# Kernel tuning notes

Hardware: AMD Instinct MI355X
Metric: run time of the kernel (lower is better)

The kernel has to match this reference:

```python
import jax, jax.numpy as jnp
import numpy as np
from jax import lax

K = 3          # kernel size
PAD = 1        # (K-1)//2
CIN = 256
COUT = 64
NSPLIT = CIN // COUT  # 4
EPS = 1e-5


def _conv2d(x, w, b):
    # x [B,C,H,W], w [O,I,K,K], b [O]
    y = lax.conv_general_dilated(x, w, (1, 1), [(PAD, PAD), (PAD, PAD)],
                                 dimension_numbers=("NCHW", "OIHW", "NCHW"))
    return y + b[None, :, None, None]


def _bilinear_sample(img, py, px):
    # img [C,H,W]; py,px [K2,H,W] absolute sample coords; zero outside borders
    H, W = img.shape[1], img.shape[2]
    y0 = jnp.floor(py)
    x0 = jnp.floor(px)
    wy1 = py - y0
    wx1 = px - x0
    wy0 = 1.0 - wy1
    wx0 = 1.0 - wx1

    def gather(yc, xc):
        valid = (yc >= 0) & (yc <= H - 1) & (xc >= 0) & (xc <= W - 1)
        yi = jnp.clip(yc, 0, H - 1).astype(jnp.int32)
        xi = jnp.clip(xc, 0, W - 1).astype(jnp.int32)
        v = img[:, yi, xi]  # [C,K2,H,W]
        return v * valid.astype(img.dtype)[None]

    return (gather(y0, x0) * (wy0 * wx0)[None]
            + gather(y0, x0 + 1.0) * (wy0 * wx1)[None]
            + gather(y0 + 1.0, x0) * (wy1 * wx0)[None]
            + gather(y0 + 1.0, x0 + 1.0) * (wy1 * wx1)[None])


def _deform_conv(x, offsets, w, b):
    # x [B,C,H,W]; offsets [B,2*K2,H,W] (torchvision layout: per kernel pt (dy,dx));
    # w [O,C,K,K]; b [O]
    B, C, H, W = x.shape
    K2 = K * K
    off = offsets.reshape(B, K2, 2, H, W)
    kh = jnp.arange(K, dtype=x.dtype)
    base_y = (jnp.arange(H, dtype=x.dtype)[None, :, None]
              + (kh[:, None] - PAD).repeat(K).reshape(K2, 1, 1))  # h + kh - pad
    base_x = (jnp.arange(W, dtype=x.dtype)[None, None, :]
              + jnp.tile(kh - PAD, K).reshape(K2, 1, 1))          # w + kw - pad
    py = base_y + off[:, :, 0]  # [B,K2,H,W]
    px = base_x + off[:, :, 1]
    sampled = jax.vmap(_bilinear_sample)(x, py, px)  # [B,C,K2,H,W]
    out = jnp.einsum("bckhw,ock->bohw", sampled, w.reshape(w.shape[0], C, K2))
    return out + b[None, :, None, None]


def setup_inputs() -> dict:
    key = jax.random.key(0)
    ks = jax.random.split(key, 10)
    B, H, W = 8, 64, 64
    x = jax.random.normal(ks[0], (B, CIN, H, W), dtype=jnp.float32)
    bn_gamma = jax.random.normal(ks[1], (CIN,), dtype=jnp.float32) * 0.1 + 1.0
    bn_beta = jax.random.normal(ks[2], (CIN,), dtype=jnp.float32) * 0.1
    bn_mean = jax.random.normal(ks[3], (CIN,), dtype=jnp.float32) * 0.1
    bn_var = jax.random.uniform(ks[4], (CIN,), dtype=jnp.float32, minval=0.5, maxval=1.5)
    offset_w = jax.random.normal(ks[5], (NSPLIT, 2 * K * K, CIN, K, K), dtype=jnp.float32) * 0.02
    offset_b = jax.random.normal(ks[6], (NSPLIT, 2 * K * K), dtype=jnp.float32) * 0.02
    dconv_w = jax.random.normal(ks[7], (NSPLIT, COUT, COUT, K, K), dtype=jnp.float32) * 0.04
    dconv_b = jax.random.normal(ks[8], (NSPLIT, COUT), dtype=jnp.float32) * 0.02
    return {"x": x, "bn_gamma": bn_gamma, "bn_beta": bn_beta, "bn_mean": bn_mean,
            "bn_var": bn_var, "offset_w": offset_w, "offset_b": offset_b,
            "dconv_w": dconv_w, "dconv_b": dconv_b}


def reference(x, bn_gamma, bn_beta, bn_mean, bn_var, offset_w, offset_b, dconv_w, dconv_b):
    # BN (eval-mode running stats) + ReLU
    inv = lax.rsqrt(bn_var + EPS)
    h = jax.nn.relu((x - bn_mean[None, :, None, None]) * (bn_gamma * inv)[None, :, None, None]
                    + bn_beta[None, :, None, None])
    out = None
    for i in range(NSPLIT):
        offsets = _conv2d(h, offset_w[i], offset_b[i])               # [B,2K2,H,W]
        x_i = h[:, i * COUT:(i + 1) * COUT]                          # [B,COUT,H,W]
        y_i = _deform_conv(x_i, offsets, dconv_w[i], dconv_b[i])
        out = y_i if out is None else out + y_i
    return out
```

## Files before the change

kernel.cpp:

```cpp
#include <hip/hip_runtime.h>

#define KK 3
#define CIN 256
#define COUT 64
#define NSPLIT 4
#define BB 8
#define HH 64
#define WW 64
#define K2 9
#define OC 18
#define EPS 1e-5f

typedef __attribute__((ext_vector_type(8))) short bf16x8;
typedef __attribute__((ext_vector_type(4))) float f32x4;
typedef __attribute__((ext_vector_type(4))) unsigned int u32x4;

#define WS_SCALE 0
#define WS_BIAS  256
#define WS_BSUM  512
#define WS_HBF   1024
#define HBF_FLOATS (BB*HH*WW*CIN/2)
#define WS_OFFS  (WS_HBF + HBF_FLOATS)
#define OFFS_SIZE (BB*72*HH*WW)
#define WS_WDT   (WS_OFFS + OFFS_SIZE)
#define WS_WOB   (WS_WDT + NSPLIT*K2*COUT*COUT/2)
#define WOB_ELEMS (K2*80*CIN)

__device__ __host__ inline unsigned short f2bf(float f) {
    unsigned int u = __builtin_bit_cast(unsigned int, f);
    unsigned int r = (u + 0x7fffu + ((u >> 16) & 1u)) >> 16;
    return (unsigned short)r;
}
__device__ inline float bf2f(unsigned short u) {
    return __builtin_bit_cast(float, (unsigned int)u << 16);
}

__global__ void prep_kernel(const float* __restrict__ g, const float* __restrict__ be,
                            const float* __restrict__ mn, const float* __restrict__ vr,
                            const float* __restrict__ db, float* __restrict__ ws) {
    int t = threadIdx.x;
    if (t < CIN) {
        float inv = 1.0f / sqrtf(vr[t] + EPS);
        float sc = g[t] * inv;
        ws[WS_SCALE + t] = sc;
        ws[WS_BIAS + t]  = be[t] - mn[t] * sc;
    }
    if (t < COUT) {
        float s = 0.f;
        for (int i = 0; i < NSPLIT; i++) s += db[i * COUT + t];
        ws[WS_BSUM + t] = s;
    }
}

__global__ void wtrans_kernel(const float* __restrict__ dw, const float* __restrict__ ow,
                              float* __restrict__ ws) {
    int tid = blockIdx.x * blockDim.x + threadIdx.x;
    if (tid < NSPLIT * K2 * COUT * COUT) {
        int cin = tid & 63;
        int o = (tid >> 6) & 63;
        int k = (tid / 4096) % 9;
        int s = tid / 36864;
        ((unsigned short*)(ws + WS_WDT))[tid] = f2bf(dw[((s * COUT + o) * COUT + cin) * 9 + k]);
    }
    if (tid < WOB_ELEMS) {
        int cin = tid & 255;
        int sc = (tid >> 8) % 80;
        int k = tid / 20480;
        unsigned short v = 0;
        if (sc < 72) {
            int s = sc / 18, c = sc % 18;
            v = f2bf(ow[((s * OC + c) * CIN + cin) * 9 + k]);
        }
        ((unsigned short*)(ws + WS_WOB))[tid] = v;
    }
}

__global__ __launch_bounds__(256) void bn_transpose_kernel(const float* __restrict__ x,
                                                           const float* __restrict__ scb,
                                                           unsigned short* __restrict__ hbf) {
    __shared__ float tile[64 * 65];
    int cg = blockIdx.x;
    int y  = blockIdx.y;
    int b  = blockIdx.z;
    int lane = threadIdx.x & 63;
    int grp  = threadIdx.x >> 6;
    #pragma unroll
    for (int i = 0; i < 16; i++) {
        int cl = grp * 16 + i;
        int c  = cg * 64 + cl;
        float v = x[((b * CIN + c) * HH + y) * WW + lane];
        float h = fmaxf(fmaf(v, scb[c], scb[256 + c]), 0.f);
        tile[cl * 65 + lane] = h;
    }
    __syncthreads();
    int cpair = threadIdx.x & 31;
    int pxg   = threadIdx.x >> 5;
    #pragma unroll
    for (int i = 0; i < 8; i++) {
        int px = pxg * 8 + i;
        unsigned int u0 = f2bf(tile[(cpair * 2) * 65 + px]);
        unsigned int u1 = f2bf(tile[(cpair * 2 + 1) * 65 + px]);
        *(unsigned int*)&hbf[((size_t)(b * HH + y) * WW + px) * CIN + cg * 64 + cpair * 2] =
            u0 | (u1 << 16);
    }
}

__global__ __launch_bounds__(256) void offconv_kernel(const unsigned short* __restrict__ hbf,
                                                      const float* __restrict__ offb,
                                                      const unsigned short* __restrict__ woB,
                                                      float* __restrict__ offs_out) {
    __shared__ unsigned short wlds[80 * 264];
    int tid = threadIdx.x;
    int bid = blockIdx.x + 64 * blockIdx.y;
    int b = bid & 7;
    int y = bid >> 3;
    int w  = tid >> 6;
    int l  = tid & 63;
    int lm = l & 15, lk = l >> 4;
    int px = w * 16 + lm;

    f32x4 acc[5];
    #pragma unroll
    for (int nt = 0; nt < 5; nt++) {
        int sc = nt * 16 + lm;
        float ob = (sc < 72) ? offb[sc] : 0.f;
        acc[nt] = (f32x4){ob, ob, ob, ob};
    }
    const unsigned short* hb = hbf + (size_t)b * HH * WW * CIN;
    const bf16x8 zero = {};

    for (int k = 0; k < 9; k++) {
        int dy = k / 3 - 1, dx = k % 3 - 1;
        int ry = y + dy;
        if ((unsigned)ry >= (unsigned)HH) continue;
        __syncthreads();
        const unsigned short* src = woB + (size_t)k * 80 * 256;
        #pragma unroll
        for (int t = 0; t < 10; t++) {
            int idx = tid + t * 256;
            int sc = idx >> 5;
            int co = (idx & 31) * 8;
            *(bf16x8*)&wlds[sc * 264 + co] = *(const bf16x8*)&src[sc * 256 + co];
        }
        __syncthreads();

        int rx = px + dx;
        bool vx = (unsigned)rx < (unsigned)WW;
        const unsigned short* arow = hb + ((size_t)ry * WW + rx) * CIN + lk * 8;
        #pragma unroll
        for (int kt = 0; kt < 8; kt++) {
            bf16x8 a = vx ? *(const bf16x8*)(arow + kt * 32) : zero;
            #pragma unroll
            for (int nt = 0; nt < 5; nt++) {
                bf16x8 bb = *(const bf16x8*)&wlds[(nt * 16 + lm) * 264 + kt * 32 + lk * 8];
                acc[nt] = __builtin_amdgcn_mfma_f32_16x16x32_bf16(a, bb, acc[nt], 0, 0, 0);
            }
        }
    }

    #pragma unroll
    for (int nt = 0; nt < 5; nt++) {
        int sc = nt * 16 + lm;
        if (sc < 72) {
            float4 v = {acc[nt][0], acc[nt][1], acc[nt][2], acc[nt][3]};
            *(float4*)&offs_out[((size_t)(b * 72 + sc) * HH + y) * WW + w * 16 + lk * 4] = v;
        }
    }
}

__global__ __launch_bounds__(512) void deform_kernel(const unsigned short* __restrict__ hbf,
                                                     const float* __restrict__ offp,
                                                     const unsigned short* __restrict__ wdT,
                                                     const float* __restrict__ bsum,
                                                     float* __restrict__ out) {
    __shared__ __align__(16) char lds[2][20480];

    int tid = threadIdx.x;
    int bid = blockIdx.x + 64 * blockIdx.y;
    int b = bid & 7;
    int y = bid >> 3;

    int h  = tid >> 8;
    int t8 = tid & 255;
    int l  = tid & 63;
    int w4 = t8 >> 6;
    int lm = l & 15;
    int lk = l >> 4;
    int pA = t8 >> 2;
    int cA = t8 & 3;
    int sub = l >> 3;
    int ch  = (l & 7) * 8;

    unsigned short* vbufS = (unsigned short*)&lds[h][0];
    unsigned short* wbufS = (unsigned short*)&lds[h][9216];
    int*            tblI  = (int*)&lds[h][18432];

    f32x4 acc[4];
    #pragma unroll
    for (int nt = 0; nt < 4; nt++) {
        float bs = h ? 0.f : bsum[nt * 16 + lm];
        acc[nt] = (f32x4){bs, bs, bs, bs};
    }

    const unsigned short* hb = hbf + (size_t)b * HH * WW * CIN;
    const float* offbase = offp + ((size_t)(b * 72 + 2 * h * 18) * HH + y) * WW + pA;

    float offy_c = offbase[0];
    float offx_c = offbase[HH * WW];

    for (int it = 0; it < 2 * K2; ++it) {
        int sl = it >= K2;
        int s  = 2 * h + sl;
        int k  = it - sl * K2;

        float offy_n = 0.f, offx_n = 0.f;
        if (it + 1 < 2 * K2) {
            int sl2 = (it + 1) >= K2;
            int k2  = (it + 1) - sl2 * K2;
            const float* oa = offbase + (size_t)(sl2 * 18 + 2 * k2) * (HH * WW);
            offy_n = oa[0];
            offx_n = oa[HH * WW];
        }

        const unsigned short* wsrc = wdT + (size_t)((s * 9 + k) * 64) * 64;
        bf16x8 wr0 = *(const bf16x8*)(wsrc + t8 * 16);
        bf16x8 wr1 = *(const bf16x8*)(wsrc + t8 * 16 + 8);

        {
            int dy = k / 3 - 1, dx = k % 3 - 1;
            float py  = (float)(y + dy) + offy_c;
            float px_ = (float)(pA + dx) + offx_c;
            float y0f = floorf(py), x0f = floorf(px_);
            float wy1 = py - y0f, wx1 = px_ - x0f;
            int yt = (int)y0f + (cA >> 1);
            int xt = (int)x0f + (cA & 1);
            float wt = ((cA >> 1) ? wy1 : 1.f - wy1) * ((cA & 1) ? wx1 : 1.f - wx1);
            bool valid = (yt >= 0) && (yt < HH) && (xt >= 0) && (xt < WW);
            wt = valid ? wt : 0.f;
            int yi = min(max(yt, 0), HH - 1);
            int xi = min(max(xt, 0), WW - 1);
            int2 e = {yi * WW + xi, __builtin_bit_cast(int, wt)};
            *(int2*)&tblI[(pA * 4 + cA) * 2] = e;
        }
        __syncthreads();

        float v0[8], v1[8];
        #pragma unroll
        for (int j = 0; j < 8; j++) { v0[j] = 0.f; v1[j] = 0.f; }
        int pg0 = w4 * 16 + sub;
        int pg1 = w4 * 16 + 8 + sub;
        #pragma unroll
        for (int c = 0; c < 4; c++) {
            int2 t0 = *(const int2*)&tblI[(pg0 * 4 + c) * 2];
            int2 t1 = *(const int2*)&tblI[(pg1 * 4 + c) * 2];
            const unsigned short* sp0 = hb + (size_t)t0.x * CIN + s * COUT + ch;
            const unsigned short* sp1 = hb + (size_t)t1.x * CIN + s * COUT + ch;
            bf16x8 d0 = *(const bf16x8*)sp0;
            bf16x8 d1 = *(const bf16x8*)sp1;
            float w0 = __builtin_bit_cast(float, t0.y);
            float w1 = __builtin_bit_cast(float, t1.y);
            #pragma unroll
            for (int j = 0; j < 8; j++) {
                v0[j] = fmaf(w0, bf2f((unsigned short)d0[j]), v0[j]);
                v1[j] = fmaf(w1, bf2f((unsigned short)d1[j]), v1[j]);
            }
        }
        {
            u32x4 q0, q1;
            #pragma unroll
            for (int j = 0; j < 4; j++) {
                q0[j] = (unsigned)f2bf(v0[2 * j]) | ((unsigned)f2bf(v0[2 * j + 1]) << 16);
                q1[j] = (unsigned)f2bf(v1[2 * j]) | ((unsigned)f2bf(v1[2 * j + 1]) << 16);
            }
            *(u32x4*)&vbufS[pg0 * 72 + ch] = q0;
            *(u32x4*)&vbufS[pg1 * 72 + ch] = q1;
        }
        {
            int wo = t8 >> 2, wpart = t8 & 3;
            *(bf16x8*)(&wbufS[wo * 72 + wpart * 16])     = wr0;
            *(bf16x8*)(&wbufS[wo * 72 + wpart * 16 + 8]) = wr1;
        }
        __syncthreads();

        #pragma unroll
        for (int ks = 0; ks < 2; ks++) {
            bf16x8 a = *(const bf16x8*)(&vbufS[(w4 * 16 + lm) * 72 + ks * 32 + lk * 8]);
            #pragma unroll
            for (int nt = 0; nt < 4; nt++) {
                bf16x8 bb = *(const bf16x8*)(&wbufS[(nt * 16 + lm) * 72 + ks * 32 + lk * 8]);
                acc[nt] = __builtin_amdgcn_mfma_f32_16x16x32_bf16(a, bb, acc[nt], 0, 0, 0);
            }
        }

        offy_c = offy_n;
        offx_c = offx_n;
    }

    __syncthreads();
    float* outT = (float*)&lds[h][0];
    #pragma unroll
    for (int nt = 0; nt < 4; nt++) {
        *(f32x4*)(&outT[(nt * 16 + lm) * 68 + w4 * 16 + lk * 4]) = acc[nt];
    }
    __syncthreads();
    {
        const float* o0 = (const float*)&lds[0][0];
        const float* o1 = (const float*)&lds[1][0];
        int o = tid >> 3, xp = (tid & 7) * 8;
        float* dst = out + (((size_t)(b * COUT + o)) * HH + y) * WW + xp;
        #pragma unroll
        for (int q = 0; q < 2; q++) {
            float4 a = *(const float4*)(&o0[o * 68 + xp + q * 4]);
            float4 c = *(const float4*)(&o1[o * 68 + xp + q * 4]);
            float4 r = {a.x + c.x, a.y + c.y, a.z + c.z, a.w + c.w};
            *(float4*)(dst + q * 4) = r;
        }
    }
}

extern "C" void kernel_launch(void* const* d_in, const int* in_sizes, int n_in,
                              void* d_out, int out_size, void* d_ws, size_t ws_size,
                              hipStream_t stream) {
    const float* x        = (const float*)d_in[0];
    const float* bn_gamma = (const float*)d_in[1];
    const float* bn_beta  = (const float*)d_in[2];
    const float* bn_mean  = (const float*)d_in[3];
    const float* bn_var   = (const float*)d_in[4];
    const float* offset_w = (const float*)d_in[5];
    const float* offset_b = (const float*)d_in[6];
    const float* dconv_w  = (const float*)d_in[7];
    const float* dconv_b  = (const float*)d_in[8];
    float* out = (float*)d_out;
    float* ws  = (float*)d_ws;

    unsigned short* hbf = (unsigned short*)(ws + WS_HBF);

    prep_kernel<<<1, 256, 0, stream>>>(bn_gamma, bn_beta, bn_mean, bn_var, dconv_b, ws);
    wtrans_kernel<<<(WOB_ELEMS + 255) / 256, 256, 0, stream>>>(dconv_w, offset_w, ws);
    bn_transpose_kernel<<<dim3(4, 64, 8), 256, 0, stream>>>(x, ws, hbf);
    offconv_kernel<<<dim3(64, 8), 256, 0, stream>>>(hbf, offset_b,
                                                    (const unsigned short*)(ws + WS_WOB),
                                                    ws + WS_OFFS);
    deform_kernel<<<dim3(64, 8), 512, 0, stream>>>(hbf, ws + WS_OFFS,
                                                   (const unsigned short*)(ws + WS_WDT),
                                                   ws + WS_BSUM, out);
}
```

Baseline: 100.3 us.

## Split deform kernel rows into half-width tiles to double block count

```diff
diff --git a/kernel.cpp b/kernel.cpp
--- a/kernel.cpp
+++ b/kernel.cpp
@@ -168,42 +168,47 @@
     }
 }
 
+#define RGN 14848
 __global__ __launch_bounds__(512) void deform_kernel(const unsigned short* __restrict__ hbf,
                                                      const float* __restrict__ offp,
                                                      const unsigned short* __restrict__ wdT,
                                                      const float* __restrict__ bsum,
                                                      float* __restrict__ out) {
-    __shared__ __align__(16) char lds[2][20480];
+    __shared__ __align__(16) char lds[2][RGN];
 
     int tid = threadIdx.x;
-    int bid = blockIdx.x + 64 * blockIdx.y;
-    int b = bid & 7;
-    int y = bid >> 3;
+    int bid = blockIdx.x + 128 * blockIdx.y;
+    int b  = bid & 7;
+    int r  = bid >> 3;
+    int y  = r >> 1;
+    int xh = r & 1;
 
     int h  = tid >> 8;
     int t8 = tid & 255;
     int l  = tid & 63;
     int w4 = t8 >> 6;
+    int wm = w4 >> 1;
+    int wn = w4 & 1;
     int lm = l & 15;
     int lk = l >> 4;
-    int pA = t8 >> 2;
+    int pA = (t8 >> 2) & 31;
     int cA = t8 & 3;
-    int sub = l >> 3;
-    int ch  = (l & 7) * 8;
+    int gp = t8 >> 3;
+    int ch = (t8 & 7) * 8;
 
     unsigned short* vbufS = (unsigned short*)&lds[h][0];
-    unsigned short* wbufS = (unsigned short*)&lds[h][9216];
-    int*            tblI  = (int*)&lds[h][18432];
-
-    f32x4 acc[4];
-    #pragma unroll
-    for (int nt = 0; nt < 4; nt++) {
-        float bs = h ? 0.f : bsum[nt * 16 + lm];
-        acc[nt] = (f32x4){bs, bs, bs, bs};
+    unsigned short* wbufS = (unsigned short*)&lds[h][4608];
+    int*            tblI  = (int*)&lds[h][13824];
+
+    f32x4 acc[2];
+    #pragma unroll
+    for (int j = 0; j < 2; j++) {
+        float bs = h ? 0.f : bsum[(wn * 2 + j) * 16 + lm];
+        acc[j] = (f32x4){bs, bs, bs, bs};
     }
 
     const unsigned short* hb = hbf + (size_t)b * HH * WW * CIN;
-    const float* offbase = offp + ((size_t)(b * 72 + 2 * h * 18) * HH + y) * WW + pA;
+    const float* offbase = offp + ((size_t)(b * 72 + 2 * h * 18) * HH + y) * WW + xh * 32 + pA;
 
     float offy_c = offbase[0];
     float offx_c = offbase[HH * WW];
@@ -229,7 +234,7 @@
         {
             int dy = k / 3 - 1, dx = k % 3 - 1;
             float py  = (float)(y + dy) + offy_c;
-            float px_ = (float)(pA + dx) + offx_c;
+            float px_ = (float)(xh * 32 + pA + dx) + offx_c;
             float y0f = floorf(py), x0f = floorf(px_);
             float wy1 = py - y0f, wx1 = px_ - x0f;
             int yt = (int)y0f + (cA >> 1);
@@ -244,36 +249,27 @@
         }
         __syncthreads();
 
-        float v0[8], v1[8];
-        #pragma unroll
-        for (int j = 0; j < 8; j++) { v0[j] = 0.f; v1[j] = 0.f; }
-        int pg0 = w4 * 16 + sub;
-        int pg1 = w4 * 16 + 8 + sub;
+        float v0[8];
+        #pragma unroll
+        for (int j = 0; j < 8; j++) v0[j] = 0.f;
         #pragma unroll
         for (int c = 0; c < 4; c++) {
-            int2 t0 = *(const int2*)&tblI[(pg0 * 4 + c) * 2];
-            int2 t1 = *(const int2*)&tblI[(pg1 * 4 + c) * 2];
+            int2 t0 = *(const int2*)&tblI[(gp * 4 + c) * 2];
             const unsigned short* sp0 = hb + (size_t)t0.x * CIN + s * COUT + ch;
-            const unsigned short* sp1 = hb + (size_t)t1.x * CIN + s * COUT + ch;
             bf16x8 d0 = *(const bf16x8*)sp0;
-            bf16x8 d1 = *(const bf16x8*)sp1;
             float w0 = __builtin_bit_cast(float, t0.y);
-            float w1 = __builtin_bit_cast(float, t1.y);
             #pragma unroll
             for (int j = 0; j < 8; j++) {
                 v0[j] = fmaf(w0, bf2f((unsigned short)d0[j]), v0[j]);
-                v1[j] = fmaf(w1, bf2f((unsigned short)d1[j]), v1[j]);
             }
         }
         {
-            u32x4 q0, q1;
+            u32x4 q0;
             #pragma unroll
             for (int j = 0; j < 4; j++) {
                 q0[j] = (unsigned)f2bf(v0[2 * j]) | ((unsigned)f2bf(v0[2 * j + 1]) << 16);
-                q1[j] = (unsigned)f2bf(v1[2 * j]) | ((unsigned)f2bf(v1[2 * j + 1]) << 16);
             }
-            *(u32x4*)&vbufS[pg0 * 72 + ch] = q0;
-            *(u32x4*)&vbufS[pg1 * 72 + ch] = q1;
+            *(u32x4*)&vbufS[gp * 72 + ch] = q0;
         }
         {
             int wo = t8 >> 2, wpart = t8 & 3;
@@ -284,11 +280,11 @@
 
         #pragma unroll
         for (int ks = 0; ks < 2; ks++) {
-            bf16x8 a = *(const bf16x8*)(&vbufS[(w4 * 16 + lm) * 72 + ks * 32 + lk * 8]);
+            bf16x8 a = *(const bf16x8*)(&vbufS[(wm * 16 + lm) * 72 + ks * 32 + lk * 8]);
             #pragma unroll
-            for (int nt = 0; nt < 4; nt++) {
-                bf16x8 bb = *(const bf16x8*)(&wbufS[(nt * 16 + lm) * 72 + ks * 32 + lk * 8]);
-                acc[nt] = __builtin_amdgcn_mfma_f32_16x16x32_bf16(a, bb, acc[nt], 0, 0, 0);
+            for (int j = 0; j < 2; j++) {
+                bf16x8 bb = *(const bf16x8*)(&wbufS[((wn * 2 + j) * 16 + lm) * 72 + ks * 32 + lk * 8]);
+                acc[j] = __builtin_amdgcn_mfma_f32_16x16x32_bf16(a, bb, acc[j], 0, 0, 0);
             }
         }
 
@@ -299,22 +295,18 @@
     __syncthreads();
     float* outT = (float*)&lds[h][0];
     #pragma unroll
-    for (int nt = 0; nt < 4; nt++) {
-        *(f32x4*)(&outT[(nt * 16 + lm) * 68 + w4 * 16 + lk * 4]) = acc[nt];
+    for (int j = 0; j < 2; j++) {
+        *(f32x4*)(&outT[((wn * 2 + j) * 16 + lm) * 36 + wm * 16 + lk * 4]) = acc[j];
     }
     __syncthreads();
     {
         const float* o0 = (const float*)&lds[0][0];
         const float* o1 = (const float*)&lds[1][0];
-        int o = tid >> 3, xp = (tid & 7) * 8;
-        float* dst = out + (((size_t)(b * COUT + o)) * HH + y) * WW + xp;
-        #pragma unroll
-        for (int q = 0; q < 2; q++) {
-            float4 a = *(const float4*)(&o0[o * 68 + xp + q * 4]);
-            float4 c = *(const float4*)(&o1[o * 68 + xp + q * 4]);
-            float4 r = {a.x + c.x, a.y + c.y, a.z + c.z, a.w + c.w};
-            *(float4*)(dst + q * 4) = r;
-        }
+        int o = tid >> 3, xq = (tid & 7) * 4;
+        float4 a = *(const float4*)(&o0[o * 36 + xq]);
+        float4 c = *(const float4*)(&o1[o * 36 + xq]);
+        float4 rr = {a.x + c.x, a.y + c.y, a.z + c.z, a.w + c.w};
+        *(float4*)(out + (((size_t)(b * COUT + o)) * HH + y) * WW + xh * 32 + xq) = rr;
     }
 }
 
@@ -341,7 +333,7 @@
     offconv_kernel<<<dim3(64, 8), 256, 0, stream>>>(hbf, offset_b,
                                                     (const unsigned short*)(ws + WS_WOB),
                                                     ws + WS_OFFS);
-    deform_kernel<<<dim3(64, 8), 512, 0, stream>>>(hbf, ws + WS_OFFS,
-                                                   (const unsigned short*)(ws + WS_WDT),
-                                                   ws + WS_BSUM, out);
-}
+    deform_kernel<<<dim3(128, 8), 512, 0, stream>>>(hbf, ws + WS_OFFS,
+                                                    (const unsigned short*)(ws + WS_WDT),
+                                                    ws + WS_BSUM, out);
+}
```

Result: no change. 101.8 us (+1.5%).

## Fuse prep kernels into one launch and XOR-swizzle deform LDS buffers

Applied to the files above, without the earlier changes.

```diff
diff --git a/kernel.cpp b/kernel.cpp
--- a/kernel.cpp
+++ b/kernel.cpp
@@ -15,8 +15,6 @@
 typedef __attribute__((ext_vector_type(4))) float f32x4;
 typedef __attribute__((ext_vector_type(4))) unsigned int u32x4;
 
-#define WS_SCALE 0
-#define WS_BIAS  256
 #define WS_BSUM  512
 #define WS_HBF   1024
 #define HBF_FLOATS (BB*HH*WW*CIN/2)
@@ -25,6 +23,8 @@
 #define WS_WDT   (WS_OFFS + OFFS_SIZE)
 #define WS_WOB   (WS_WDT + NSPLIT*K2*COUT*COUT/2)
 #define WOB_ELEMS (K2*80*CIN)
+#define NBN_BLOCKS 2048
+#define NWT_BLOCKS ((WOB_ELEMS + 255) / 256)
 
 __device__ __host__ inline unsigned short f2bf(float f) {
     unsigned int u = __builtin_bit_cast(unsigned int, f);
@@ -35,73 +35,78 @@
     return __builtin_bit_cast(float, (unsigned int)u << 16);
 }
 
-__global__ void prep_kernel(const float* __restrict__ g, const float* __restrict__ be,
-                            const float* __restrict__ mn, const float* __restrict__ vr,
-                            const float* __restrict__ db, float* __restrict__ ws) {
-    int t = threadIdx.x;
-    if (t < CIN) {
-        float inv = 1.0f / sqrtf(vr[t] + EPS);
-        float sc = g[t] * inv;
-        ws[WS_SCALE + t] = sc;
-        ws[WS_BIAS + t]  = be[t] - mn[t] * sc;
-    }
-    if (t < COUT) {
-        float s = 0.f;
-        for (int i = 0; i < NSPLIT; i++) s += db[i * COUT + t];
-        ws[WS_BSUM + t] = s;
-    }
-}
-
-__global__ void wtrans_kernel(const float* __restrict__ dw, const float* __restrict__ ow,
-                              float* __restrict__ ws) {
-    int tid = blockIdx.x * blockDim.x + threadIdx.x;
-    if (tid < NSPLIT * K2 * COUT * COUT) {
-        int cin = tid & 63;
-        int o = (tid >> 6) & 63;
-        int k = (tid / 4096) % 9;
-        int s = tid / 36864;
-        ((unsigned short*)(ws + WS_WDT))[tid] = f2bf(dw[((s * COUT + o) * COUT + cin) * 9 + k]);
-    }
-    if (tid < WOB_ELEMS) {
-        int cin = tid & 255;
-        int sc = (tid >> 8) % 80;
-        int k = tid / 20480;
-        unsigned short v = 0;
-        if (sc < 72) {
-            int s = sc / 18, c = sc % 18;
-            v = f2bf(ow[((s * OC + c) * CIN + cin) * 9 + k]);
-        }
-        ((unsigned short*)(ws + WS_WOB))[tid] = v;
-    }
-}
-
-__global__ __launch_bounds__(256) void bn_transpose_kernel(const float* __restrict__ x,
-                                                           const float* __restrict__ scb,
-                                                           unsigned short* __restrict__ hbf) {
-    __shared__ float tile[64 * 65];
-    int cg = blockIdx.x;
-    int y  = blockIdx.y;
-    int b  = blockIdx.z;
-    int lane = threadIdx.x & 63;
-    int grp  = threadIdx.x >> 6;
-    #pragma unroll
-    for (int i = 0; i < 16; i++) {
-        int cl = grp * 16 + i;
-        int c  = cg * 64 + cl;
-        float v = x[((b * CIN + c) * HH + y) * WW + lane];
-        float h = fmaxf(fmaf(v, scb[c], scb[256 + c]), 0.f);
-        tile[cl * 65 + lane] = h;
-    }
-    __syncthreads();
-    int cpair = threadIdx.x & 31;
-    int pxg   = threadIdx.x >> 5;
-    #pragma unroll
-    for (int i = 0; i < 8; i++) {
-        int px = pxg * 8 + i;
-        unsigned int u0 = f2bf(tile[(cpair * 2) * 65 + px]);
-        unsigned int u1 = f2bf(tile[(cpair * 2 + 1) * 65 + px]);
-        *(unsigned int*)&hbf[((size_t)(b * HH + y) * WW + px) * CIN + cg * 64 + cpair * 2] =
-            u0 | (u1 << 16);
+__global__ __launch_bounds__(256) void prep_kernel(const float* __restrict__ x,
+                                                   const float* __restrict__ g,
+                                                   const float* __restrict__ be,
+                                                   const float* __restrict__ mn,
+                                                   const float* __restrict__ vr,
+                                                   const float* __restrict__ dw,
+                                                   const float* __restrict__ ow,
+                                                   const float* __restrict__ db,
+                                                   float* __restrict__ ws,
+                                                   unsigned short* __restrict__ hbf) {
+    if (blockIdx.x < NBN_BLOCKS) {
+        __shared__ float tile[64 * 65];
+        __shared__ float scl[64], bil[64];
+        int bid = blockIdx.x;
+        int cg = bid & 3;
+        int y  = (bid >> 2) & 63;
+        int b  = bid >> 8;
+        int t = threadIdx.x;
+        if (t < 64) {
+            int c = cg * 64 + t;
+            float inv = rsqrtf(vr[c] + EPS);
+            float sc = g[c] * inv;
+            scl[t] = sc;
+            bil[t] = be[c] - mn[c] * sc;
+        }
+        __syncthreads();
+        int lane = t & 63;
+        int grp  = t >> 6;
+        #pragma unroll
+        for (int i = 0; i < 16; i++) {
+            int cl = grp * 16 + i;
+            int c  = cg * 64 + cl;
+            float v = x[((b * CIN + c) * HH + y) * WW + lane];
+            float h = fmaxf(fmaf(v, scl[cl], bil[cl]), 0.f);
+            tile[cl * 65 + lane] = h;
+        }
+        __syncthreads();
+        int cpair = t & 31;
+        int pxg   = t >> 5;
+        #pragma unroll
+        for (int i = 0; i < 8; i++) {
+            int px = pxg * 8 + i;
+            unsigned int u0 = f2bf(tile[(cpair * 2) * 65 + px]);
+            unsigned int u1 = f2bf(tile[(cpair * 2 + 1) * 65 + px]);
+            *(unsigned int*)&hbf[((size_t)(b * HH + y) * WW + px) * CIN + cg * 64 + cpair * 2] =
+                u0 | (u1 << 16);
+        }
+    } else {
+        int tid = (blockIdx.x - NBN_BLOCKS) * 256 + threadIdx.x;
+        if (blockIdx.x == NBN_BLOCKS && threadIdx.x < COUT) {
+            float s = 0.f;
+            for (int i = 0; i < NSPLIT; i++) s += db[i * COUT + threadIdx.x];
+            ws[WS_BSUM + threadIdx.x] = s;
+        }
+        if (tid < NSPLIT * K2 * COUT * COUT) {
+            int cin = tid & 63;
+            int o = (tid >> 6) & 63;
+            int k = (tid / 4096) % 9;
+            int s = tid / 36864;
+            ((unsigned short*)(ws + WS_WDT))[tid] = f2bf(dw[((s * COUT + o) * COUT + cin) * 9 + k]);
+        }
+        if (tid < WOB_ELEMS) {
+            int cin = tid & 255;
+            int sc = (tid >> 8) % 80;
+            int k = tid / 20480;
+            unsigned short v = 0;
+            if (sc < 72) {
+                int s = sc / 18, c = sc % 18;
+                v = f2bf(ow[((s * OC + c) * CIN + cin) * 9 + k]);
+            }
+            ((unsigned short*)(ws + WS_WOB))[tid] = v;
+        }
     }
 }
 
@@ -168,12 +173,13 @@
     }
 }
 
-__global__ __launch_bounds__(512) void deform_kernel(const unsigned short* __restrict__ hbf,
-                                                     const float* __restrict__ offp,
-                                                     const unsigned short* __restrict__ wdT,
-                                                     const float* __restrict__ bsum,
-                                                     float* __restrict__ out) {
-    __shared__ __align__(16) char lds[2][20480];
+#define RGN 18432
+__global__ __launch_bounds__(512, 4) void deform_kernel(const unsigned short* __restrict__ hbf,
+                                                        const float* __restrict__ offp,
+                                                        const unsigned short* __restrict__ wdT,
+                                                        const float* __restrict__ bsum,
+                                                        float* __restrict__ out) {
+    __shared__ __align__(16) char lds[2][RGN];
 
     int tid = threadIdx.x;
     int bid = blockIdx.x + 64 * blockIdx.y;
@@ -189,11 +195,12 @@
     int pA = t8 >> 2;
     int cA = t8 & 3;
     int sub = l >> 3;
-    int ch  = (l & 7) * 8;
-
-    unsigned short* vbufS = (unsigned short*)&lds[h][0];
-    unsigned short* wbufS = (unsigned short*)&lds[h][9216];
-    int*            tblI  = (int*)&lds[h][18432];
+    int chq = l & 7;
+
+    char* half_ = lds[h];
+    char* vbufB = half_;
+    char* wbufB = half_ + 8192;
+    int2* tbl2  = (int2*)(half_ + 16384);
 
     f32x4 acc[4];
     #pragma unroll
@@ -239,56 +246,60 @@
             wt = valid ? wt : 0.f;
             int yi = min(max(yt, 0), HH - 1);
             int xi = min(max(xt, 0), WW - 1);
-            int2 e = {yi * WW + xi, __builtin_bit_cast(int, wt)};
-            *(int2*)&tblI[(pA * 4 + cA) * 2] = e;
-        }
-        __syncthreads();
-
-        float v0[8], v1[8];
-        #pragma unroll
-        for (int j = 0; j < 8; j++) { v0[j] = 0.f; v1[j] = 0.f; }
-        int pg0 = w4 * 16 + sub;
-        int pg1 = w4 * 16 + 8 + sub;
-        #pragma unroll
-        for (int c = 0; c < 4; c++) {
-            int2 t0 = *(const int2*)&tblI[(pg0 * 4 + c) * 2];
-            int2 t1 = *(const int2*)&tblI[(pg1 * 4 + c) * 2];
-            const unsigned short* sp0 = hb + (size_t)t0.x * CIN + s * COUT + ch;
-            const unsigned short* sp1 = hb + (size_t)t1.x * CIN + s * COUT + ch;
-            bf16x8 d0 = *(const bf16x8*)sp0;
-            bf16x8 d1 = *(const bf16x8*)sp1;
-            float w0 = __builtin_bit_cast(float, t0.y);
-            float w1 = __builtin_bit_cast(float, t1.y);
-            #pragma unroll
-            for (int j = 0; j < 8; j++) {
-                v0[j] = fmaf(w0, bf2f((unsigned short)d0[j]), v0[j]);
-                v1[j] = fmaf(w1, bf2f((unsigned short)d1[j]), v1[j]);
-            }
-        }
+            tbl2[pA * 4 + cA] = (int2){yi * WW + xi, __builtin_bit_cast(int, wt)};
+        }
+        __syncthreads();
+
         {
+            int pg0 = w4 * 16 + sub;
+            int pg1 = pg0 + 8;
+            float v0[8], v1[8];
+            #pragma unroll
+            for (int j = 0; j < 8; j++) { v0[j] = 0.f; v1[j] = 0.f; }
+            const unsigned short* sb = hb + s * COUT + chq * 8;
+            #pragma unroll
+            for (int c = 0; c < 4; c++) {
+                int2 t0 = tbl2[pg0 * 4 + c];
+                int2 t1 = tbl2[pg1 * 4 + c];
+                bf16x8 d0 = *(const bf16x8*)(sb + (size_t)t0.x * CIN);
+                bf16x8 d1 = *(const bf16x8*)(sb + (size_t)t1.x * CIN);
+                float w0 = __builtin_bit_cast(float, t0.y);
+                float w1 = __builtin_bit_cast(float, t1.y);
+                #pragma unroll
+                for (int j = 0; j < 8; j++) {
+                    v0[j] = fmaf(w0, bf2f((unsigned short)d0[j]), v0[j]);
+                    v1[j] = fmaf(w1, bf2f((unsigned short)d1[j]), v1[j]);
+                }
+            }
             u32x4 q0, q1;
             #pragma unroll
             for (int j = 0; j < 4; j++) {
                 q0[j] = (unsigned)f2bf(v0[2 * j]) | ((unsigned)f2bf(v0[2 * j + 1]) << 16);
                 q1[j] = (unsigned)f2bf(v1[2 * j]) | ((unsigned)f2bf(v1[2 * j + 1]) << 16);
             }
-            *(u32x4*)&vbufS[pg0 * 72 + ch] = q0;
-            *(u32x4*)&vbufS[pg1 * 72 + ch] = q1;
+            *(u32x4*)(vbufB + pg0 * 128 + ((chq * 16) ^ ((pg0 & 7) << 4))) = q0;
+            *(u32x4*)(vbufB + pg1 * 128 + ((chq * 16) ^ ((pg1 & 7) << 4))) = q1;
         }
         {
-            int wo = t8 >> 2, wpart = t8 & 3;
-            *(bf16x8*)(&wbufS[wo * 72 + wpart * 16])     = wr0;
-            *(bf16x8*)(&wbufS[wo * 72 + wpart * 16 + 8]) = wr1;
-        }
-        __syncthreads();
-
-        #pragma unroll
-        for (int ks = 0; ks < 2; ks++) {
-            bf16x8 a = *(const bf16x8*)(&vbufS[(w4 * 16 + lm) * 72 + ks * 32 + lk * 8]);
-            #pragma unroll
-            for (int nt = 0; nt < 4; nt++) {
-                bf16x8 bb = *(const bf16x8*)(&wbufS[(nt * 16 + lm) * 72 + ks * 32 + lk * 8]);
-                acc[nt] = __builtin_amdgcn_mfma_f32_16x16x32_bf16(a, bb, acc[nt], 0, 0, 0);
+            int wo = t8 >> 2, wq = t8 & 3;
+            int sw = (wo & 7) << 4;
+            *(bf16x8*)(wbufB + wo * 128 + ((wq * 32) ^ sw))      = wr0;
+            *(bf16x8*)(wbufB + wo * 128 + ((wq * 32 + 16) ^ sw)) = wr1;
+        }
+        __syncthreads();
+
+        {
+            int aswz = (lm & 7) << 4;
+            #pragma unroll
+            for (int ks = 0; ks < 2; ks++) {
+                bf16x8 a = *(const bf16x8*)(vbufB + (w4 * 16 + lm) * 128 +
+                                            ((ks * 64 + lk * 16) ^ aswz));
+                #pragma unroll
+                for (int nt = 0; nt < 4; nt++) {
+                    bf16x8 bb = *(const bf16x8*)(wbufB + (nt * 16 + lm) * 128 +
+                                                 ((ks * 64 + lk * 16) ^ aswz));
+                    acc[nt] = __builtin_amdgcn_mfma_f32_16x16x32_bf16(a, bb, acc[nt], 0, 0, 0);
+                }
             }
         }
 
@@ -297,23 +308,23 @@
     }
 
     __syncthreads();
-    float* outT = (float*)&lds[h][0];
+    float* outT = (float*)half_;
     #pragma unroll
     for (int nt = 0; nt < 4; nt++) {
         *(f32x4*)(&outT[(nt * 16 + lm) * 68 + w4 * 16 + lk * 4]) = acc[nt];
     }
     __syncthreads();
     {
-        const float* o0 = (const float*)&lds[0][0];
-        const float* o1 = (const float*)&lds[1][0];
+        const float* o0 = (const float*)lds[0];
+        const float* o1 = (const float*)lds[1];
         int o = tid >> 3, xp = (tid & 7) * 8;
         float* dst = out + (((size_t)(b * COUT + o)) * HH + y) * WW + xp;
         #pragma unroll
         for (int q = 0; q < 2; q++) {
             float4 a = *(const float4*)(&o0[o * 68 + xp + q * 4]);
             float4 c = *(const float4*)(&o1[o * 68 + xp + q * 4]);
-            float4 r = {a.x + c.x, a.y + c.y, a.z + c.z, a.w + c.w};
-            *(float4*)(dst + q * 4) = r;
+            float4 rr = {a.x + c.x, a.y + c.y, a.z + c.z, a.w + c.w};
+            *(float4*)(dst + q * 4) = rr;
         }
     }
 }
@@ -335,9 +346,9 @@
 
     unsigned short* hbf = (unsigned short*)(ws + WS_HBF);
 
-    prep_kernel<<<1, 256, 0, stream>>>(bn_gamma, bn_beta, bn_mean, bn_var, dconv_b, ws);
-    wtrans_kernel<<<(WOB_ELEMS + 255) / 256, 256, 0, stream>>>(dconv_w, offset_w, ws);
-    bn_transpose_kernel<<<dim3(4, 64, 8), 256, 0, stream>>>(x, ws, hbf);
+    prep_kernel<<<NBN_BLOCKS + NWT_BLOCKS, 256, 0, stream>>>(x, bn_gamma, bn_beta, bn_mean,
+                                                             bn_var, dconv_w, offset_w,
+                                                             dconv_b, ws, hbf);
     offconv_kernel<<<dim3(64, 8), 256, 0, stream>>>(hbf, offset_b,
                                                     (const unsigned short*)(ws + WS_WOB),
                                                     ws + WS_OFFS);
```

Result: faster. 86.04 us (-14.2%).
